# Performance work log

Measured on AMD Instinct MI355X. Metric: run time of the kernel, lower is better.

The kernel has to match this reference:

```python
import jax, jax.numpy as jnp
import numpy as np

B, N, D = 8, 2048, 128

def setup_inputs() -> dict:
    key = jax.random.key(0)
    k1, k2, k3 = jax.random.split(key, 3)
    h = jax.random.normal(k1, (B, N, D), dtype=jnp.float32)
    W = jax.random.normal(k2, (D, D), dtype=jnp.float32) * (1.0 / np.sqrt(D))
    # a has shape [1,1,1,2D] in torch; flatten to [2D] (xavier-normal init)
    a = jax.random.normal(k3, (2 * D,), dtype=jnp.float32) * np.sqrt(2.0 / (2 * D))
    return {"h": h, "W": W, "a": a}

def reference(h, W, a):
    act = jax.nn.relu
    # h <- h @ W^T (nn.Linear with weight W means x @ W.T; here W is the weight matrix)
    hw = jnp.einsum('bnd,ed->bne', h, W)  # [B,N,D]
    a_i, a_j = a[:D], a[D:]
    # e_ij = act(a_i . h_i + a_j . h_j) -- equivalent to sum(cat(h_i,h_j)*a, -1)
    s_i = jnp.einsum('bnd,d->bn', hw, a_i)  # [B,N]
    s_j = jnp.einsum('bnd,d->bn', hw, a_j)  # [B,N]
    e = act(s_i[:, :, None] + s_j[:, None, :])  # [B,N,N]
    a_ij = jax.nn.softmax(e, axis=2)
    out = act(jnp.einsum('bij,bjd->bid', a_ij, hw))
    return out
```

## Files before the change

kernel.cpp:

```cpp
#include <hip/hip_runtime.h>
#include <hip/hip_bf16.h>

#define BB 8
#define NN 2048
#define DD 128
#define TI 32
#define HP 132
#define CH 32
#define NC (NN / CH)
#define NO (NC + 1)
#define NFIX (BB * NO)
#define OG 16
#define RB 128

__device__ __forceinline__ float relu(float x) { return x > 0.f ? x : 0.f; }

typedef __attribute__((ext_vector_type(8))) __bf16 bf16x8;
typedef __attribute__((ext_vector_type(4))) float f32x4;

__device__ __forceinline__ void cvt2(float x, __bf16& hi, __bf16& lo) {
    hi = (__bf16)x;
    lo = (__bf16)(x - (float)hi);
}

__global__ __launch_bounds__(256) void GraphAttentionalLayer_1168231104632_kernel(
    const float* __restrict__ h,
    const float* __restrict__ W,
    const float* __restrict__ a,
    float* __restrict__ hw,
    float* __restrict__ E,
    float* __restrict__ F)
{
    __shared__ float hw_s[TI][HP];

    const int tid = threadIdx.x;
    const int lane = tid & 63;
    const int w  = tid >> 6;
    const int wm = w & 1;
    const int wn = w >> 1;
    const int lr = lane & 15;
    const int kg = lane >> 4;
    const int b  = blockIdx.x >> 6;
    const int i0 = (blockIdx.x & 63) * TI;

    const int arow = i0 + wm * 16 + lr;
    const float* hrow = h + ((size_t)b * NN + arow) * DD;

    f32x4 acc[4];
#pragma unroll
    for (int nf = 0; nf < 4; nf++) acc[nf] = (f32x4){0.f, 0.f, 0.f, 0.f};

#pragma unroll
    for (int kc = 0; kc < 4; kc++) {
        const int kb = kc * 32 + kg * 8;
        const float4 av0 = *reinterpret_cast<const float4*>(hrow + kb);
        const float4 av1 = *reinterpret_cast<const float4*>(hrow + kb + 4);
        const float av[8] = {av0.x, av0.y, av0.z, av0.w, av1.x, av1.y, av1.z, av1.w};
        bf16x8 ah, al;
#pragma unroll
        for (int e = 0; e < 8; e++) { __bf16 hi, lo; cvt2(av[e], hi, lo); ah[e] = hi; al[e] = lo; }

#pragma unroll
        for (int nf = 0; nf < 4; nf++) {
            const int wr = wn * 64 + nf * 16 + lr;
            const float* wrow = W + (size_t)wr * DD + kb;
            const float4 bv0 = *reinterpret_cast<const float4*>(wrow);
            const float4 bv1 = *reinterpret_cast<const float4*>(wrow + 4);
            const float bv[8] = {bv0.x, bv0.y, bv0.z, bv0.w, bv1.x, bv1.y, bv1.z, bv1.w};
            bf16x8 bh, bl;
#pragma unroll
            for (int e = 0; e < 8; e++) { __bf16 hi, lo; cvt2(bv[e], hi, lo); bh[e] = hi; bl[e] = lo; }

            acc[nf] = __builtin_amdgcn_mfma_f32_16x16x32_bf16(ah, bh, acc[nf], 0, 0, 0);
            acc[nf] = __builtin_amdgcn_mfma_f32_16x16x32_bf16(ah, bl, acc[nf], 0, 0, 0);
            acc[nf] = __builtin_amdgcn_mfma_f32_16x16x32_bf16(al, bh, acc[nf], 0, 0, 0);
        }
    }

#pragma unroll
    for (int nf = 0; nf < 4; nf++)
#pragma unroll
        for (int r = 0; r < 4; r++)
            hw_s[wm * 16 + kg * 4 + r][wn * 64 + nf * 16 + lr] = acc[nf][r];
    __syncthreads();

    const int row = tid >> 3;
    const int cb  = (tid & 7) * 4;
    const size_t gbase = ((size_t)b * NN + i0 + row) * DD;
    float pi = 0.f, pj = 0.f;
#pragma unroll
    for (int qq = 0; qq < 4; qq++) {
        const int col = cb + qq * 32;
        const float4 v = *reinterpret_cast<const float4*>(&hw_s[row][col]);
        *reinterpret_cast<float4*>(&hw[gbase + col]) = v;
        const float4 avi = *reinterpret_cast<const float4*>(&a[col]);
        const float4 avj = *reinterpret_cast<const float4*>(&a[DD + col]);
        pi += v.x * avi.x + v.y * avi.y + v.z * avi.z + v.w * avi.w;
        pj += v.x * avj.x + v.y * avj.y + v.z * avj.z + v.w * avj.w;
    }
#pragma unroll
    for (int off = 4; off > 0; off >>= 1) {
        pi += __shfl_down(pi, off, 8);
        pj += __shfl_down(pj, off, 8);
    }
    if ((tid & 7) == 0) {
        const size_t rr = (size_t)b * NN + i0 + row;
        E[rr] = __expf(pi);
        F[rr] = __expf(pj);
    }
}

__global__ __launch_bounds__(256) void GraphAttentionalLayer_1168231104632_rank(
    const float* __restrict__ F,
    float* __restrict__ Fsorted,
    int* __restrict__ perm)
{
    __shared__ float F_s[NN];
    __shared__ int   part[16][16];

    const int t = threadIdx.x;
    const int b = blockIdx.x >> 7;
    const int j0 = (blockIdx.x & (RB - 1)) * 16;
    const size_t nb = (size_t)b * NN;

    for (int q = 0; q < NN / 256; q++)
        F_s[q * 256 + t] = F[nb + q * 256 + t];
    __syncthreads();

    const int tj = t & 15, ts = t >> 4;
    const int j = j0 + tj;
    const float fj = F_s[j];
    const int m0 = ts * (NN / 16);
    int cnt = 0;
    const float4* F4 = reinterpret_cast<const float4*>(&F_s[m0]);
#pragma unroll 8
    for (int mi4 = 0; mi4 < NN / 64; mi4++) {
        const float4 fm4 = F4[mi4];
        const int m = m0 + mi4 * 4;
        cnt += (fm4.x < fj) | ((fm4.x == fj) & (m     < j));
        cnt += (fm4.y < fj) | ((fm4.y == fj) & (m + 1 < j));
        cnt += (fm4.z < fj) | ((fm4.z == fj) & (m + 2 < j));
        cnt += (fm4.w < fj) | ((fm4.w == fj) & (m + 3 < j));
    }
    part[ts][tj] = cnt;
    __syncthreads();
    if (ts == 0) {
        int r = 0;
#pragma unroll
        for (int s = 0; s < 16; s++) r += part[s][tj];
        Fsorted[nb + r] = fj;
        perm[nb + r] = j;
    }
}

__global__ __launch_bounds__(128) void GraphAttentionalLayer_1168231104632_scan(
    const float* __restrict__ hw,
    const float* __restrict__ Fsorted,
    const int* __restrict__ perm,
    float* __restrict__ Q0L, float* __restrict__ Q1L,
    float* __restrict__ C0,  float* __restrict__ C1)
{
    const int t = threadIdx.x;
    const int b = blockIdx.x / NC, c = blockIdx.x % NC;
    const size_t nb = (size_t)b * NN;
    const int m0 = c * CH;

    int   jv[CH];
    float Fv[CH];
#pragma unroll
    for (int mm = 0; mm < CH; mm++) jv[mm] = perm[nb + m0 + mm];
#pragma unroll
    for (int mm = 0; mm < CH; mm++) Fv[mm] = Fsorted[nb + m0 + mm];

    float hv[CH];
#pragma unroll
    for (int mm = 0; mm < CH; mm++)
        hv[mm] = hw[(nb + jv[mm]) * DD + t];

    float a0 = 0.f, a1 = 0.f;
#pragma unroll
    for (int mm = 0; mm < CH; mm++) {
        const int m = m0 + mm;
        Q0L[(nb + m) * DD + t] = a0;
        Q1L[(nb + m) * DD + t] = a1;
        a0 += hv[mm];
        a1 += Fv[mm] * hv[mm];
    }
    C0[((size_t)b * NC + c) * DD + t] = a0;
    C1[((size_t)b * NC + c) * DD + t] = a1;
}

__global__ __launch_bounds__(256) void GraphAttentionalLayer_1168231104632_mid(
    const float* __restrict__ C0, const float* __restrict__ C1,
    const float* __restrict__ Fsorted, const float* __restrict__ E,
    float* __restrict__ O0, float* __restrict__ O1,
    int* __restrict__ kk,  float* __restrict__ zinv)
{
    __shared__ float fs_s[NN];
    __shared__ float cf_s[NC];
    __shared__ float of_s[NO];

    const int tid = threadIdx.x;

    if (blockIdx.x < NFIX) {
        const int b = blockIdx.x / NO, c = blockIdx.x % NO;
        const int d = tid & 127;
        const float* C = (tid < 128) ? C0 : C1;
        float*       O = (tid < 128) ? O0 : O1;
        float o = 0.f;
        int c2 = 0;
        for (; c2 + 16 <= c; c2 += 16) {
            float v[16];
#pragma unroll
            for (int q = 0; q < 16; q++)
                v[q] = C[((size_t)b * NC + c2 + q) * DD + d];
#pragma unroll
            for (int q = 0; q < 16; q++) o += v[q];
        }
        for (; c2 < c; c2++)
            o += C[((size_t)b * NC + c2) * DD + d];
        O[((size_t)b * NO + c) * DD + d] = o;
        return;
    }

    const int sb = blockIdx.x - NFIX;
    const int b = sb >> 3;
    const int i0 = (sb & 7) * 256;
    const size_t nb = (size_t)b * NN;

    for (int q = 0; q < NN / 256; q++)
        fs_s[q * 256 + tid] = Fsorted[nb + q * 256 + tid];
    __syncthreads();

    if (tid < NC) {
        float p = 0.f;
        const int m0 = tid * CH;
#pragma unroll
        for (int mm = 0; mm < CH; mm++) p += fs_s[m0 + mm];
        cf_s[tid] = p;
    }
    __syncthreads();
    if (tid < NO) {
        float p = 0.f;
        for (int c2 = 0; c2 < tid; c2++) p += cf_s[c2];
        of_s[tid] = p;
    }
    __syncthreads();

    const int row = (int)nb + i0 + tid;
    const float Ei = E[row];
    const float thr = 1.0f / Ei;
    int lo = 0, hi = NN;
    while (lo < hi) {
        const int mid = (lo + hi) >> 1;
        if (fs_s[mid] < thr) lo = mid + 1; else hi = mid;
    }
    float fpl = 0.f;
    for (int m = (lo >> 5) << 5; m < lo; m++) fpl += fs_s[m];
    const float TF = of_s[NC];
    const float Pk = of_s[lo >> 5] + fpl;
    const float z = Ei * (TF - Pk) + (float)lo;
    kk[row] = lo;
    zinv[row] = 1.0f / z;
}

__global__ __launch_bounds__(256) void GraphAttentionalLayer_1168231104632_out(
    const float* __restrict__ Q0L, const float* __restrict__ Q1L,
    const float* __restrict__ O0,  const float* __restrict__ O1,
    const int* __restrict__ kk,    const float* __restrict__ zinv,
    const float* __restrict__ E,   float* __restrict__ out)
{
    const int tid = threadIdx.x;
    const int t  = tid & 127;
    const int rp = tid >> 7;
    const int r0 = blockIdx.x * OG;
    const int b  = r0 >> 11;
    const size_t nb = (size_t)b * NN;
    const float* O0b = O0 + (size_t)b * NO * DD;
    const float* O1b = O1 + (size_t)b * NO * DD;

    const float T1  = O1b[(size_t)NC * DD + t];
    const float TQ0 = O0b[(size_t)NC * DD + t];

#pragma unroll
    for (int q = 0; q < OG / 2; q++) {
        const int row = r0 + q * 2 + rp;
        const int k = kk[row];
        const float Ev = E[row];
        const float zv = zinv[row];

        float num;
        if (k < NN) {
            const int c = k >> 5;
            const float q0 = Q0L[(nb + k) * DD + t] + O0b[(size_t)c * DD + t];
            const float q1 = Q1L[(nb + k) * DD + t] + O1b[(size_t)c * DD + t];
            num = Ev * (T1 - q1) + q0;
        } else {
            num = TQ0;
        }
        out[(size_t)row * DD + t] = relu(num * zv);
    }
}

extern "C" __attribute__((visibility("default")))
void kernel_launch(void* const* d_in, const int* in_sizes, int n_in,
                   void* d_out, int out_size, void* d_ws, size_t ws_size,
                   hipStream_t stream) {
    const float* h = nullptr; const float* W = nullptr; const float* a = nullptr;
    for (int i = 0; i < n_in; i++) {
        if (in_sizes[i] == BB * NN * DD)      h = (const float*)d_in[i];
        else if (in_sizes[i] == DD * DD)      W = (const float*)d_in[i];
        else if (in_sizes[i] == 2 * DD)       a = (const float*)d_in[i];
    }
    if (!h) h = (const float*)d_in[0];
    if (!W) W = (const float*)d_in[1];
    if (!a) a = (const float*)d_in[2];

    float* out = (float*)d_out;
    float* ws = (float*)d_ws;

    float* hw   = ws;
    float* E    = hw + (size_t)BB * NN * DD;
    float* F    = E + BB * NN;
    float* Fs   = F + BB * NN;
    float* zinv = Fs + BB * NN;
    int*   perm = (int*)(zinv + BB * NN);
    int*   kk   = perm + BB * NN;
    float* Q0L  = (float*)(kk + BB * NN);
    float* Q1L  = Q0L + (size_t)BB * NN * DD;
    float* C0   = Q1L + (size_t)BB * NN * DD;
    float* C1   = C0 + BB * NC * DD;
    float* O0   = C1 + BB * NC * DD;
    float* O1   = O0 + BB * NO * DD;
    const size_t need = (size_t)((O1 + BB * NO * DD) - ws) * sizeof(float);

    if (ws_size < need || d_ws == nullptr) {
        hipMemsetAsync(d_out, 0x42, (size_t)out_size * sizeof(float), stream);
        return;
    }

    GraphAttentionalLayer_1168231104632_kernel<<<BB * (NN / TI), 256, 0, stream>>>(h, W, a, hw, E, F);
    GraphAttentionalLayer_1168231104632_rank<<<BB * RB, 256, 0, stream>>>(F, Fs, perm);
    GraphAttentionalLayer_1168231104632_scan<<<BB * NC, 128, 0, stream>>>(hw, Fs, perm, Q0L, Q1L, C0, C1);
    GraphAttentionalLayer_1168231104632_mid<<<NFIX + BB * 8, 256, 0, stream>>>(C0, C1, Fs, E, O0, O1, kk, zinv);
    GraphAttentionalLayer_1168231104632_out<<<(BB * NN) / OG, 256, 0, stream>>>(Q0L, Q1L, O0, O1, kk, zinv, E, out);
}
```

Before: 99.66 us.

## Fold a into W for scores and fuse hw GEMM into sorted scan

The first kernel no longer computes hw. It computes u = W^T a_i and v = W^T a_j per block and takes the scores directly as h·u and h·v. The hw GEMM moves into the scan kernel, which gathers the permuted h rows and runs the MFMA split-bf16 product there, then does the prefix scan from shared memory. This removes the hw global write and the gathered re-read. In exchange, every block recomputes W^T a with a serial 128-step loop, and the scores now follow a different floating-point summation order.

```diff
diff --git a/kernel.cpp b/kernel.cpp
--- a/kernel.cpp
+++ b/kernel.cpp
@@ -4,7 +4,6 @@
 #define BB 8
 #define NN 2048
 #define DD 128
-#define TI 32
 #define HP 132
 #define CH 32
 #define NC (NN / CH)
@@ -27,76 +26,40 @@
     const float* __restrict__ h,
     const float* __restrict__ W,
     const float* __restrict__ a,
-    float* __restrict__ hw,
     float* __restrict__ E,
     float* __restrict__ F)
 {
-    __shared__ float hw_s[TI][HP];
+    __shared__ float u_s[DD];
+    __shared__ float v_s[DD];
 
     const int tid = threadIdx.x;
-    const int lane = tid & 63;
-    const int w  = tid >> 6;
-    const int wm = w & 1;
-    const int wn = w >> 1;
-    const int lr = lane & 15;
-    const int kg = lane >> 4;
     const int b  = blockIdx.x >> 6;
-    const int i0 = (blockIdx.x & 63) * TI;
-
-    const int arow = i0 + wm * 16 + lr;
-    const float* hrow = h + ((size_t)b * NN + arow) * DD;
-
-    f32x4 acc[4];
-#pragma unroll
-    for (int nf = 0; nf < 4; nf++) acc[nf] = (f32x4){0.f, 0.f, 0.f, 0.f};
-
-#pragma unroll
-    for (int kc = 0; kc < 4; kc++) {
-        const int kb = kc * 32 + kg * 8;
-        const float4 av0 = *reinterpret_cast<const float4*>(hrow + kb);
-        const float4 av1 = *reinterpret_cast<const float4*>(hrow + kb + 4);
-        const float av[8] = {av0.x, av0.y, av0.z, av0.w, av1.x, av1.y, av1.z, av1.w};
-        bf16x8 ah, al;
-#pragma unroll
-        for (int e = 0; e < 8; e++) { __bf16 hi, lo; cvt2(av[e], hi, lo); ah[e] = hi; al[e] = lo; }
-
-#pragma unroll
-        for (int nf = 0; nf < 4; nf++) {
-            const int wr = wn * 64 + nf * 16 + lr;
-            const float* wrow = W + (size_t)wr * DD + kb;
-            const float4 bv0 = *reinterpret_cast<const float4*>(wrow);
-            const float4 bv1 = *reinterpret_cast<const float4*>(wrow + 4);
-            const float bv[8] = {bv0.x, bv0.y, bv0.z, bv0.w, bv1.x, bv1.y, bv1.z, bv1.w};
-            bf16x8 bh, bl;
-#pragma unroll
-            for (int e = 0; e < 8; e++) { __bf16 hi, lo; cvt2(bv[e], hi, lo); bh[e] = hi; bl[e] = lo; }
-
-            acc[nf] = __builtin_amdgcn_mfma_f32_16x16x32_bf16(ah, bh, acc[nf], 0, 0, 0);
-            acc[nf] = __builtin_amdgcn_mfma_f32_16x16x32_bf16(ah, bl, acc[nf], 0, 0, 0);
-            acc[nf] = __builtin_amdgcn_mfma_f32_16x16x32_bf16(al, bh, acc[nf], 0, 0, 0);
-        }
-    }
-
-#pragma unroll
-    for (int nf = 0; nf < 4; nf++)
-#pragma unroll
-        for (int r = 0; r < 4; r++)
-            hw_s[wm * 16 + kg * 4 + r][wn * 64 + nf * 16 + lr] = acc[nf][r];
+    const int i0 = (blockIdx.x & 63) * 32;
+    const size_t nb = (size_t)b * NN;
+
+    {
+        const int d = tid & 127;
+        const float* av = (tid < DD) ? a : (a + DD);
+        float acc = 0.f;
+#pragma unroll 16
+        for (int e = 0; e < DD; e++)
+            acc += av[e] * W[(size_t)e * DD + d];
+        if (tid < DD) u_s[d] = acc; else v_s[d] = acc;
+    }
     __syncthreads();
 
     const int row = tid >> 3;
     const int cb  = (tid & 7) * 4;
-    const size_t gbase = ((size_t)b * NN + i0 + row) * DD;
+    const float* hrow = h + (nb + i0 + row) * DD;
     float pi = 0.f, pj = 0.f;
 #pragma unroll
-    for (int qq = 0; qq < 4; qq++) {
-        const int col = cb + qq * 32;
-        const float4 v = *reinterpret_cast<const float4*>(&hw_s[row][col]);
-        *reinterpret_cast<float4*>(&hw[gbase + col]) = v;
-        const float4 avi = *reinterpret_cast<const float4*>(&a[col]);
-        const float4 avj = *reinterpret_cast<const float4*>(&a[DD + col]);
-        pi += v.x * avi.x + v.y * avi.y + v.z * avi.z + v.w * avi.w;
-        pj += v.x * avj.x + v.y * avj.y + v.z * avj.z + v.w * avj.w;
+    for (int q = 0; q < 4; q++) {
+        const int col = cb + q * 32;
+        const float4 hv = *reinterpret_cast<const float4*>(&hrow[col]);
+        const float4 uu = *reinterpret_cast<const float4*>(&u_s[col]);
+        const float4 vv = *reinterpret_cast<const float4*>(&v_s[col]);
+        pi += hv.x * uu.x + hv.y * uu.y + hv.z * uu.z + hv.w * uu.w;
+        pj += hv.x * vv.x + hv.y * vv.y + hv.z * vv.z + hv.w * vv.w;
     }
 #pragma unroll
     for (int off = 4; off > 0; off >>= 1) {
@@ -104,9 +67,8 @@
         pj += __shfl_down(pj, off, 8);
     }
     if ((tid & 7) == 0) {
-        const size_t rr = (size_t)b * NN + i0 + row;
-        E[rr] = __expf(pi);
-        F[rr] = __expf(pj);
+        E[nb + i0 + row] = __expf(pi);
+        F[nb + i0 + row] = __expf(pj);
     }
 }
 
@@ -153,41 +115,87 @@
     }
 }
 
-__global__ __launch_bounds__(128) void GraphAttentionalLayer_1168231104632_scan(
-    const float* __restrict__ hw,
+__global__ __launch_bounds__(256) void GraphAttentionalLayer_1168231104632_scan(
+    const float* __restrict__ h,
+    const float* __restrict__ W,
     const float* __restrict__ Fsorted,
     const int* __restrict__ perm,
     float* __restrict__ Q0L, float* __restrict__ Q1L,
     float* __restrict__ C0,  float* __restrict__ C1)
 {
-    const int t = threadIdx.x;
-    const int b = blockIdx.x / NC, c = blockIdx.x % NC;
+    __shared__ float hw_s[CH][HP];
+    __shared__ float fs_sh[CH];
+
+    const int tid = threadIdx.x;
+    const int lane = tid & 63;
+    const int w  = tid >> 6;
+    const int wm = w & 1;
+    const int wn = w >> 1;
+    const int lr = lane & 15;
+    const int kg = lane >> 4;
+    const int b  = blockIdx.x >> 6;
+    const int c  = blockIdx.x & 63;
     const size_t nb = (size_t)b * NN;
     const int m0 = c * CH;
 
-    int   jv[CH];
-    float Fv[CH];
-#pragma unroll
-    for (int mm = 0; mm < CH; mm++) jv[mm] = perm[nb + m0 + mm];
-#pragma unroll
-    for (int mm = 0; mm < CH; mm++) Fv[mm] = Fsorted[nb + m0 + mm];
-
-    float hv[CH];
-#pragma unroll
-    for (int mm = 0; mm < CH; mm++)
-        hv[mm] = hw[(nb + jv[mm]) * DD + t];
-
-    float a0 = 0.f, a1 = 0.f;
-#pragma unroll
-    for (int mm = 0; mm < CH; mm++) {
-        const int m = m0 + mm;
-        Q0L[(nb + m) * DD + t] = a0;
-        Q1L[(nb + m) * DD + t] = a1;
-        a0 += hv[mm];
-        a1 += Fv[mm] * hv[mm];
-    }
-    C0[((size_t)b * NC + c) * DD + t] = a0;
-    C1[((size_t)b * NC + c) * DD + t] = a1;
+    if (tid < CH) fs_sh[tid] = Fsorted[nb + m0 + tid];
+
+    const int arow = wm * 16 + lr;
+    const int jrow = perm[nb + m0 + arow];
+    const float* hrow = h + (nb + jrow) * DD;
+
+    f32x4 acc[4];
+#pragma unroll
+    for (int nf = 0; nf < 4; nf++) acc[nf] = (f32x4){0.f, 0.f, 0.f, 0.f};
+
+#pragma unroll
+    for (int kc = 0; kc < 4; kc++) {
+        const int kb = kc * 32 + kg * 8;
+        const float4 av0 = *reinterpret_cast<const float4*>(hrow + kb);
+        const float4 av1 = *reinterpret_cast<const float4*>(hrow + kb + 4);
+        const float av[8] = {av0.x, av0.y, av0.z, av0.w, av1.x, av1.y, av1.z, av1.w};
+        bf16x8 ah, al;
+#pragma unroll
+        for (int e = 0; e < 8; e++) { __bf16 hi, lo; cvt2(av[e], hi, lo); ah[e] = hi; al[e] = lo; }
+
+#pragma unroll
+        for (int nf = 0; nf < 4; nf++) {
+            const int wr = wn * 64 + nf * 16 + lr;
+            const float* wrow = W + (size_t)wr * DD + kb;
+            const float4 bv0 = *reinterpret_cast<const float4*>(wrow);
+            const float4 bv1 = *reinterpret_cast<const float4*>(wrow + 4);
+            const float bv[8] = {bv0.x, bv0.y, bv0.z, bv0.w, bv1.x, bv1.y, bv1.z, bv1.w};
+            bf16x8 bh, bl;
+#pragma unroll
+            for (int e = 0; e < 8; e++) { __bf16 hi, lo; cvt2(bv[e], hi, lo); bh[e] = hi; bl[e] = lo; }
+
+            acc[nf] = __builtin_amdgcn_mfma_f32_16x16x32_bf16(ah, bh, acc[nf], 0, 0, 0);
+            acc[nf] = __builtin_amdgcn_mfma_f32_16x16x32_bf16(ah, bl, acc[nf], 0, 0, 0);
+            acc[nf] = __builtin_amdgcn_mfma_f32_16x16x32_bf16(al, bh, acc[nf], 0, 0, 0);
+        }
+    }
+
+#pragma unroll
+    for (int nf = 0; nf < 4; nf++)
+#pragma unroll
+        for (int r = 0; r < 4; r++)
+            hw_s[wm * 16 + kg * 4 + r][wn * 64 + nf * 16 + lr] = acc[nf][r];
+    __syncthreads();
+
+    if (tid < DD) {
+        const int t = tid;
+        float a0 = 0.f, a1 = 0.f;
+#pragma unroll
+        for (int mm = 0; mm < CH; mm++) {
+            const float hv = hw_s[mm][t];
+            Q0L[(nb + m0 + mm) * DD + t] = a0;
+            Q1L[(nb + m0 + mm) * DD + t] = a1;
+            a0 += hv;
+            a1 += fs_sh[mm] * hv;
+        }
+        C0[((size_t)b * NC + c) * DD + t] = a0;
+        C1[((size_t)b * NC + c) * DD + t] = a1;
+    }
 }
 
 __global__ __launch_bounds__(256) void GraphAttentionalLayer_1168231104632_mid(
@@ -339,9 +347,9 @@
         return;
     }
 
-    GraphAttentionalLayer_1168231104632_kernel<<<BB * (NN / TI), 256, 0, stream>>>(h, W, a, hw, E, F);
+    GraphAttentionalLayer_1168231104632_kernel<<<BB * 64, 256, 0, stream>>>(h, W, a, E, F);
     GraphAttentionalLayer_1168231104632_rank<<<BB * RB, 256, 0, stream>>>(F, Fs, perm);
-    GraphAttentionalLayer_1168231104632_scan<<<BB * NC, 128, 0, stream>>>(hw, Fs, perm, Q0L, Q1L, C0, C1);
+    GraphAttentionalLayer_1168231104632_scan<<<BB * NC, 256, 0, stream>>>(h, W, Fs, perm, Q0L, Q1L, C0, C1);
     GraphAttentionalLayer_1168231104632_mid<<<NFIX + BB * 8, 256, 0, stream>>>(C0, C1, Fs, E, O0, O1, kk, zinv);
     GraphAttentionalLayer_1168231104632_out<<<(BB * NN) / OG, 256, 0, stream>>>(Q0L, Q1L, O0, O1, kk, zinv, E, out);
 }
```

New measurement: 103.2 us. +3.5%, slower.
